# Kernel optimization log

Hardware: AMD Instinct MI355X
Metric: run time of the kernel (lower is better)

## Reference

```python
import jax, jax.numpy as jnp
import numpy as np

B, D, H = 512, 256, 512

def setup_inputs() -> dict:
    key = jax.random.key(0)
    ks = jax.random.split(key, 7)
    s = lambda fan_in: 1.0 / np.sqrt(fan_in)
    return {
        "h": jax.random.normal(ks[0], (B, D), jnp.float32),
        "W1": jax.random.normal(ks[1], (2 * D, H), jnp.float32) * s(2 * D),
        "b1": jax.random.normal(ks[2], (H,), jnp.float32) * s(2 * D),
        "W2": jax.random.normal(ks[3], (H, H), jnp.float32) * s(H),
        "b2": jax.random.normal(ks[4], (H,), jnp.float32) * s(H),
        "W3": jax.random.normal(ks[5], (H, 1), jnp.float32) * s(H),
        "b3": jax.random.normal(ks[6], (1,), jnp.float32) * s(H),
    }

def reference(h, W1, b1, W2, b2, W3, b3):
    n = h.shape[0]
    # Split W1 into halves acting on hi and hj; equivalent to cat([hi,hj]) @ W1
    yi = h @ W1[:D]            # [B, H]
    yj = h @ W1[D:]            # [B, H]
    x = jnp.tanh(yi[:, None, :] + yj[None, :, :] + b1)   # [B, B, H]
    x = jnp.tanh(x @ W2 + b2)                             # [B, B, H]
    logits = (x @ W3 + b3)[..., 0]                        # [B, B]
    eye = jnp.eye(n, dtype=logits.dtype)
    return logits * (1.0 - eye) + (-20.0) * eye
```

## Files before the change

kernel.cpp:

```cpp
#include <hip/hip_runtime.h>
#include <hip/hip_bf16.h>
#include <cstdint>


#define NB 512
#define ND 256
#define NH 512
#define C2 2.885390081777927f

typedef int i32x4 __attribute__((ext_vector_type(4)));
typedef int i32x16 __attribute__((ext_vector_type(16)));
typedef unsigned int u32;
typedef unsigned char u8;

__device__ __forceinline__ float exp2_fast(float x) {
#if __has_builtin(__builtin_amdgcn_exp2f)
  return __builtin_amdgcn_exp2f(x);
#else
  return exp2f(x);
#endif
}
__device__ __forceinline__ float rcp_fast(float x) {
#if __has_builtin(__builtin_amdgcn_rcpf)
  return __builtin_amdgcn_rcpf(x);
#else
  return 1.0f / x;
#endif
}
__device__ __forceinline__ float tanh_pre(float u) {
  return fmaf(-2.0f, rcp_fast(exp2_fast(u) + 1.0f), 1.0f);
}
__device__ __forceinline__ int tanh_q127(float u) {
  return (int)rintf(fmaf(-254.0f, rcp_fast(exp2_fast(u) + 1.0f), 127.0f));
}

__global__ __launch_bounds__(256) void prep_all(const float* __restrict__ h,
                                                const float* __restrict__ W1,
                                                const float* __restrict__ b1,
                                                const float* __restrict__ W2,
                                                float* __restrict__ Ai,
                                                float* __restrict__ Aj,
                                                u8* __restrict__ W2q) {
  const int t = threadIdx.x;
  if (blockIdx.x < 128) {
    __shared__ float hs[4][ND];
    const int i0 = blockIdx.x * 4;
    for (int idx = t; idx < 4 * ND; idx += 256) hs[idx >> 8][idx & 255] = h[i0 * ND + idx];
    __syncthreads();
    float ai0[4] = {0, 0, 0, 0}, ai1[4] = {0, 0, 0, 0};
    float aj0[4] = {0, 0, 0, 0}, aj1[4] = {0, 0, 0, 0};
#pragma unroll 4
    for (int d = 0; d < ND; ++d) {
      const float wA0 = W1[d * NH + t];
      const float wA1 = W1[d * NH + t + 256];
      const float wB0 = W1[(d + ND) * NH + t];
      const float wB1 = W1[(d + ND) * NH + t + 256];
#pragma unroll
      for (int r = 0; r < 4; ++r) {
        const float hd = hs[r][d];
        ai0[r] = fmaf(hd, wA0, ai0[r]);
        ai1[r] = fmaf(hd, wA1, ai1[r]);
        aj0[r] = fmaf(hd, wB0, aj0[r]);
        aj1[r] = fmaf(hd, wB1, aj1[r]);
      }
    }
    const float b1a = b1[t], b1b = b1[t + 256];
#pragma unroll
    for (int r = 0; r < 4; ++r) {
      const int i = i0 + r;
      Ai[i * NH + t] = ai0[r] * C2;
      Ai[i * NH + t + 256] = ai1[r] * C2;
      Aj[i * NH + t] = (aj0[r] + b1a) * C2;
      Aj[i * NH + t + 256] = (aj1[r] + b1b) * C2;
    }
  } else {
    const int g = (blockIdx.x - 128) * 256 + t;
    const int lane = g & 63;
    const int nt = (g >> 6) & 15;
    const int ks = g >> 10;
    const int n = nt * 32 + (lane & 31);
    const int kb = ks * 32 + ((lane >> 5) << 4);
    u32 w[4];
#pragma unroll
    for (int q = 0; q < 4; ++q) {
      u32 acc = 0;
#pragma unroll
      for (int j = 0; j < 4; ++j) {
        const float wv = fminf(fmaxf(W2[(kb + q * 4 + j) * NH + n], -0.25f), 0.25f);
        const int qi = (int)rintf(wv * 508.0f);
        acc |= ((u32)(qi & 255)) << (8 * j);
      }
      w[q] = acc;
    }
    ((uint4*)W2q)[g] = make_uint4(w[0], w[1], w[2], w[3]);
  }
}

__global__ __launch_bounds__(512, 4) void pair_main(const float* __restrict__ Ai,
                                                    const float* __restrict__ Aj,
                                                    const u8* __restrict__ W2q,
                                                    const float* __restrict__ b2,
                                                    const float* __restrict__ W3,
                                                    const float* __restrict__ b3,
                                                    float* __restrict__ out) {
  __shared__ __align__(16) u8 xs[64 * 512];
  __shared__ float red[8][32];

  const int t = threadIdx.x;
  const int w = t >> 6;
  const int lane = t & 63;
  const int lhi = lane >> 5;
  const int llo = lane & 31;
  const int mt = w >> 2;
  const int ng = w & 3;
  const int bx = blockIdx.x;
  const int i = bx >> 3;
  const int j0 = (bx & 7) * 64;

  i32x16 acc[4];
#pragma unroll
  for (int nt = 0; nt < 4; ++nt)
#pragma unroll
    for (int q = 0; q < 16; ++q) acc[nt][q] = 0;

  {
    const float* ajr = Aj + (size_t)(j0 + lane) * NH;
    const float* air = Ai + (size_t)i * NH;
#pragma unroll
    for (int u = 0; u < 4; ++u) {
      const int s = w + u * 8;
      const int k0 = s * 16;
      u32 pk[4];
#pragma unroll
      for (int q = 0; q < 4; ++q) {
        const float4 fa = *(const float4*)(ajr + k0 + q * 4);
        const float4 ga = *(const float4*)(air + k0 + q * 4);
        const int q0 = tanh_q127(fa.x + ga.x);
        const int q1 = tanh_q127(fa.y + ga.y);
        const int q2 = tanh_q127(fa.z + ga.z);
        const int q3 = tanh_q127(fa.w + ga.w);
        pk[q] = ((u32)(q0 & 255)) | ((u32)(q1 & 255) << 8) |
                ((u32)(q2 & 255) << 16) | ((u32)(q3 & 255) << 24);
      }
      ((uint4*)xs)[s * 64 + lane] = make_uint4(pk[0], pk[1], pk[2], pk[3]);
    }
  }
  __syncthreads();

  const i32x4* xsv = (const i32x4*)xs;
  const int aslot = lhi * 64 + mt * 32 + llo;
  const uint4* w2v = (const uint4*)W2q + ng * 256 + lane;

  i32x4 a = xsv[aslot];
  uint4 b0 = w2v[0], b1 = w2v[64], b2r = w2v[128], b3r = w2v[192];

#pragma unroll 2
  for (int ks = 0; ks < 16; ++ks) {
    i32x4 na;
    uint4 nb0, nb1, nb2, nb3;
    if (ks < 15) {
      na = xsv[(ks + 1) * 128 + aslot];
      const uint4* wp = w2v + (ks + 1) * 1024;
      nb0 = wp[0]; nb1 = wp[64]; nb2 = wp[128]; nb3 = wp[192];
    }
    acc[0] = __builtin_amdgcn_mfma_i32_32x32x32_i8(a, __builtin_bit_cast(i32x4, b0), acc[0], 0, 0, 0);
    acc[1] = __builtin_amdgcn_mfma_i32_32x32x32_i8(a, __builtin_bit_cast(i32x4, b1), acc[1], 0, 0, 0);
    acc[2] = __builtin_amdgcn_mfma_i32_32x32x32_i8(a, __builtin_bit_cast(i32x4, b2r), acc[2], 0, 0, 0);
    acc[3] = __builtin_amdgcn_mfma_i32_32x32x32_i8(a, __builtin_bit_cast(i32x4, b3r), acc[3], 0, 0, 0);
    a = na;
    b0 = nb0; b1 = nb1; b2r = nb2; b3r = nb3;
  }

  const float SCALE = (0.25f / (127.0f * 127.0f)) * C2;
  float b2c[4], w3v[4];
#pragma unroll
  for (int ntl = 0; ntl < 4; ++ntl) {
    const int n = ng * 128 + ntl * 32 + llo;
    b2c[ntl] = b2[n] * C2;
    w3v[ntl] = W3[n];
  }
#pragma unroll
  for (int reg = 0; reg < 16; ++reg) {
    float s = 0.0f;
#pragma unroll
    for (int ntl = 0; ntl < 4; ++ntl)
      s += tanh_pre(fmaf((float)acc[ntl][reg], SCALE, b2c[ntl])) * w3v[ntl];
#pragma unroll
    for (int off = 1; off < 32; off <<= 1) s += __shfl_xor(s, off, 64);
    const int row = (reg & 3) + 8 * (reg >> 2) + 4 * lhi;
    if (llo == reg) red[w][row] = s;
  }
  __syncthreads();
  if (t < 64) {
    const int g0 = (t >> 5) * 4;
    const int r = t & 31;
    const float v = red[g0][r] + red[g0 + 1][r] + red[g0 + 2][r] + red[g0 + 3][r] + b3[0];
    const int j = j0 + t;
    out[i * NB + j] = (j == i) ? -20.0f : v;
  }
}

extern "C" void kernel_launch(void* const* d_in, const int* in_sizes, int n_in,
                              void* d_out, int out_size, void* d_ws, size_t ws_size,
                              hipStream_t stream) {
  const float* h = (const float*)d_in[0];
  const float* W1 = (const float*)d_in[1];
  const float* b1 = (const float*)d_in[2];
  const float* W2 = (const float*)d_in[3];
  const float* b2 = (const float*)d_in[4];
  const float* W3 = (const float*)d_in[5];
  const float* b3 = (const float*)d_in[6];
  float* out = (float*)d_out;

  float* Ai = (float*)d_ws;
  float* Aj = Ai + NB * NH;
  u8* W2q = (u8*)(Aj + NB * NH);

  prep_all<<<192, 256, 0, stream>>>(h, W1, b1, W2, Ai, Aj, W2q);
  pair_main<<<4096, 512, 0, stream>>>(Ai, Aj, W2q, b2, W3, b3, out);
}
```

Baseline: 268.8 us.

## Shrink pair tile to 32 rows, magic-number int8 packing, folded tanh epilogue

The main kernel now handles 32 j-rows per block instead of 64, with each of 8 waves owning 64 output columns. That halves LDS use and allows 6 blocks per CU, at the cost of reloading W2q twice as often. The int8 quantization of tanh uses a float magic-constant add plus byte-permute packing instead of rint and shifts. The epilogue folds the constant part of tanh into a precomputed sum of W3, and W2 fragments are double-buffered two steps ahead. The prep kernel also splits its W1 projection across twice as many blocks.

```diff
diff --git a/kernel.cpp b/kernel.cpp
--- a/kernel.cpp
+++ b/kernel.cpp
@@ -27,11 +27,22 @@
   return 1.0f / x;
 #endif
 }
-__device__ __forceinline__ float tanh_pre(float u) {
-  return fmaf(-2.0f, rcp_fast(exp2_fast(u) + 1.0f), 1.0f);
-}
-__device__ __forceinline__ int tanh_q127(float u) {
-  return (int)rintf(fmaf(-254.0f, rcp_fast(exp2_fast(u) + 1.0f), 127.0f));
+__device__ __forceinline__ u32 perm_b32(u32 hi, u32 lo, u32 sel) {
+#if __has_builtin(__builtin_amdgcn_perm)
+  return __builtin_amdgcn_perm(hi, lo, sel);
+#else
+  u32 r = 0;
+  for (int b = 0; b < 4; ++b) {
+    const u32 c = (sel >> (8 * b)) & 255;
+    const u32 byte = (c < 4) ? (lo >> (8 * c)) & 255 : (c < 8) ? (hi >> (8 * (c - 4))) & 255 : 0;
+    r |= byte << (8 * b);
+  }
+  return r;
+#endif
+}
+__device__ __forceinline__ u32 tanh_q127_magic(float u) {
+  const float r = rcp_fast(exp2_fast(u) + 1.0f);
+  return __builtin_bit_cast(u32, fmaf(-254.0f, r, 12583039.0f));
 }
 
 __global__ __launch_bounds__(256) void prep_all(const float* __restrict__ h,
@@ -42,39 +53,33 @@
                                                 float* __restrict__ Aj,
                                                 u8* __restrict__ W2q) {
   const int t = threadIdx.x;
-  if (blockIdx.x < 128) {
+  const int bx = blockIdx.x;
+  if (bx < 256) {
     __shared__ float hs[4][ND];
-    const int i0 = blockIdx.x * 4;
+    const int i0 = (bx >> 1) * 4;
+    const int n = (bx & 1) * 256 + t;
     for (int idx = t; idx < 4 * ND; idx += 256) hs[idx >> 8][idx & 255] = h[i0 * ND + idx];
     __syncthreads();
-    float ai0[4] = {0, 0, 0, 0}, ai1[4] = {0, 0, 0, 0};
-    float aj0[4] = {0, 0, 0, 0}, aj1[4] = {0, 0, 0, 0};
-#pragma unroll 4
+    float ai[4] = {0, 0, 0, 0}, aj[4] = {0, 0, 0, 0};
+#pragma unroll 8
     for (int d = 0; d < ND; ++d) {
-      const float wA0 = W1[d * NH + t];
-      const float wA1 = W1[d * NH + t + 256];
-      const float wB0 = W1[(d + ND) * NH + t];
-      const float wB1 = W1[(d + ND) * NH + t + 256];
+      const float wA = W1[d * NH + n];
+      const float wB = W1[(d + ND) * NH + n];
 #pragma unroll
       for (int r = 0; r < 4; ++r) {
         const float hd = hs[r][d];
-        ai0[r] = fmaf(hd, wA0, ai0[r]);
-        ai1[r] = fmaf(hd, wA1, ai1[r]);
-        aj0[r] = fmaf(hd, wB0, aj0[r]);
-        aj1[r] = fmaf(hd, wB1, aj1[r]);
+        ai[r] = fmaf(hd, wA, ai[r]);
+        aj[r] = fmaf(hd, wB, aj[r]);
       }
     }
-    const float b1a = b1[t], b1b = b1[t + 256];
+    const float b1n = b1[n];
 #pragma unroll
     for (int r = 0; r < 4; ++r) {
-      const int i = i0 + r;
-      Ai[i * NH + t] = ai0[r] * C2;
-      Ai[i * NH + t + 256] = ai1[r] * C2;
-      Aj[i * NH + t] = (aj0[r] + b1a) * C2;
-      Aj[i * NH + t + 256] = (aj1[r] + b1b) * C2;
+      Ai[(i0 + r) * NH + n] = ai[r] * C2;
+      Aj[(i0 + r) * NH + n] = (aj[r] + b1n) * C2;
     }
   } else {
-    const int g = (blockIdx.x - 128) * 256 + t;
+    const int g = (bx - 256) * 256 + t;
     const int lane = g & 63;
     const int nt = (g >> 6) & 15;
     const int ks = g >> 10;
@@ -96,14 +101,14 @@
   }
 }
 
-__global__ __launch_bounds__(512, 4) void pair_main(const float* __restrict__ Ai,
+__global__ __launch_bounds__(512, 6) void pair_main(const float* __restrict__ Ai,
                                                     const float* __restrict__ Aj,
                                                     const u8* __restrict__ W2q,
                                                     const float* __restrict__ b2,
                                                     const float* __restrict__ W3,
                                                     const float* __restrict__ b3,
                                                     float* __restrict__ out) {
-  __shared__ __align__(16) u8 xs[64 * 512];
+  __shared__ __align__(16) u8 xs[32 * 512];
   __shared__ float red[8][32];
 
   const int t = threadIdx.x;
@@ -111,90 +116,99 @@
   const int lane = t & 63;
   const int lhi = lane >> 5;
   const int llo = lane & 31;
-  const int mt = w >> 2;
-  const int ng = w & 3;
   const int bx = blockIdx.x;
-  const int i = bx >> 3;
-  const int j0 = (bx & 7) * 64;
-
-  i32x16 acc[4];
-#pragma unroll
-  for (int nt = 0; nt < 4; ++nt)
+  const int i = bx >> 4;
+  const int j0 = (bx & 15) * 32;
+
+  i32x16 acc[2];
+#pragma unroll
+  for (int nt = 0; nt < 2; ++nt)
 #pragma unroll
     for (int q = 0; q < 16; ++q) acc[nt][q] = 0;
 
   {
-    const float* ajr = Aj + (size_t)(j0 + lane) * NH;
+    const int row = t & 31;
+    const int s0 = t >> 5;
+    const float* ajr = Aj + (size_t)(j0 + row) * NH;
     const float* air = Ai + (size_t)i * NH;
 #pragma unroll
-    for (int u = 0; u < 4; ++u) {
-      const int s = w + u * 8;
+    for (int uu = 0; uu < 2; ++uu) {
+      const int s = s0 + uu * 16;
       const int k0 = s * 16;
-      u32 pk[4];
+      u32 wds[4];
 #pragma unroll
       for (int q = 0; q < 4; ++q) {
         const float4 fa = *(const float4*)(ajr + k0 + q * 4);
         const float4 ga = *(const float4*)(air + k0 + q * 4);
-        const int q0 = tanh_q127(fa.x + ga.x);
-        const int q1 = tanh_q127(fa.y + ga.y);
-        const int q2 = tanh_q127(fa.z + ga.z);
-        const int q3 = tanh_q127(fa.w + ga.w);
-        pk[q] = ((u32)(q0 & 255)) | ((u32)(q1 & 255) << 8) |
-                ((u32)(q2 & 255) << 16) | ((u32)(q3 & 255) << 24);
+        const u32 m0 = tanh_q127_magic(fa.x + ga.x);
+        const u32 m1 = tanh_q127_magic(fa.y + ga.y);
+        const u32 m2 = tanh_q127_magic(fa.z + ga.z);
+        const u32 m3 = tanh_q127_magic(fa.w + ga.w);
+        const u32 p01 = perm_b32(m1, m0, 0x0C0C0400u);
+        const u32 p23 = perm_b32(m3, m2, 0x0C0C0400u);
+        wds[q] = perm_b32(p23, p01, 0x05040100u);
       }
-      ((uint4*)xs)[s * 64 + lane] = make_uint4(pk[0], pk[1], pk[2], pk[3]);
+      ((uint4*)xs)[s * 32 + row] = make_uint4(wds[0], wds[1], wds[2], wds[3]);
     }
   }
   __syncthreads();
 
   const i32x4* xsv = (const i32x4*)xs;
-  const int aslot = lhi * 64 + mt * 32 + llo;
-  const uint4* w2v = (const uint4*)W2q + ng * 256 + lane;
-
-  i32x4 a = xsv[aslot];
-  uint4 b0 = w2v[0], b1 = w2v[64], b2r = w2v[128], b3r = w2v[192];
-
-#pragma unroll 2
+  const int abase = lhi * 32 + llo;
+  const uint4* w2v = (const uint4*)W2q + w * 128 + lane;
+
+  i32x4 a = xsv[abase];
+  uint4 b00 = w2v[0], b01 = w2v[64];
+  uint4 b10 = w2v[1024], b11 = w2v[1024 + 64];
+
+#pragma unroll 4
   for (int ks = 0; ks < 16; ++ks) {
-    i32x4 na;
-    uint4 nb0, nb1, nb2, nb3;
-    if (ks < 15) {
-      na = xsv[(ks + 1) * 128 + aslot];
-      const uint4* wp = w2v + (ks + 1) * 1024;
-      nb0 = wp[0]; nb1 = wp[64]; nb2 = wp[128]; nb3 = wp[192];
-    }
-    acc[0] = __builtin_amdgcn_mfma_i32_32x32x32_i8(a, __builtin_bit_cast(i32x4, b0), acc[0], 0, 0, 0);
-    acc[1] = __builtin_amdgcn_mfma_i32_32x32x32_i8(a, __builtin_bit_cast(i32x4, b1), acc[1], 0, 0, 0);
-    acc[2] = __builtin_amdgcn_mfma_i32_32x32x32_i8(a, __builtin_bit_cast(i32x4, b2r), acc[2], 0, 0, 0);
-    acc[3] = __builtin_amdgcn_mfma_i32_32x32x32_i8(a, __builtin_bit_cast(i32x4, b3r), acc[3], 0, 0, 0);
+    uint4 nb0 = make_uint4(0, 0, 0, 0), nb1 = nb0;
+    i32x4 na = {0, 0, 0, 0};
+    if (ks < 14) {
+      const uint4* wp = w2v + (ks + 2) * 1024;
+      nb0 = wp[0];
+      nb1 = wp[64];
+    }
+    if (ks < 15) na = xsv[(ks + 1) * 64 + abase];
+    acc[0] = __builtin_amdgcn_mfma_i32_32x32x32_i8(a, __builtin_bit_cast(i32x4, b00), acc[0], 0, 0, 0);
+    acc[1] = __builtin_amdgcn_mfma_i32_32x32x32_i8(a, __builtin_bit_cast(i32x4, b01), acc[1], 0, 0, 0);
     a = na;
-    b0 = nb0; b1 = nb1; b2r = nb2; b3r = nb3;
+    b00 = b10; b01 = b11;
+    b10 = nb0; b11 = nb1;
   }
 
   const float SCALE = (0.25f / (127.0f * 127.0f)) * C2;
-  float b2c[4], w3v[4];
-#pragma unroll
-  for (int ntl = 0; ntl < 4; ++ntl) {
-    const int n = ng * 128 + ntl * 32 + llo;
+  float b2c[2], w3v[2];
+#pragma unroll
+  for (int ntl = 0; ntl < 2; ++ntl) {
+    const int n = w * 64 + ntl * 32 + llo;
     b2c[ntl] = b2[n] * C2;
     w3v[ntl] = W3[n];
   }
+  float w3s = w3v[0] + w3v[1];
+#pragma unroll
+  for (int off = 1; off < 32; off <<= 1) w3s += __shfl_xor(w3s, off, 64);
+
 #pragma unroll
   for (int reg = 0; reg < 16; ++reg) {
-    float s = 0.0f;
-#pragma unroll
-    for (int ntl = 0; ntl < 4; ++ntl)
-      s += tanh_pre(fmaf((float)acc[ntl][reg], SCALE, b2c[ntl])) * w3v[ntl];
-#pragma unroll
-    for (int off = 1; off < 32; off <<= 1) s += __shfl_xor(s, off, 64);
+    float sr = 0.0f;
+#pragma unroll
+    for (int ntl = 0; ntl < 2; ++ntl) {
+      const float y = fmaf((float)acc[ntl][reg], SCALE, b2c[ntl]);
+      const float r = rcp_fast(exp2_fast(y) + 1.0f);
+      sr = fmaf(w3v[ntl], r, sr);
+    }
+#pragma unroll
+    for (int off = 1; off < 32; off <<= 1) sr += __shfl_xor(sr, off, 64);
     const int row = (reg & 3) + 8 * (reg >> 2) + 4 * lhi;
-    if (llo == reg) red[w][row] = s;
+    if (llo == reg) red[w][row] = fmaf(-2.0f, sr, w3s);
   }
   __syncthreads();
-  if (t < 64) {
-    const int g0 = (t >> 5) * 4;
-    const int r = t & 31;
-    const float v = red[g0][r] + red[g0 + 1][r] + red[g0 + 2][r] + red[g0 + 3][r] + b3[0];
+  if (t < 32) {
+    float v = b3[0];
+#pragma unroll
+    for (int ww = 0; ww < 8; ++ww) v += red[ww][t];
     const int j = j0 + t;
     out[i * NB + j] = (j == i) ? -20.0f : v;
   }
@@ -216,6 +230,6 @@
   float* Aj = Ai + NB * NH;
   u8* W2q = (u8*)(Aj + NB * NH);
 
-  prep_all<<<192, 256, 0, stream>>>(h, W1, b1, W2, Ai, Aj, W2q);
-  pair_main<<<4096, 512, 0, stream>>>(Ai, Aj, W2q, b2, W3, b3, out);
-}
+  prep_all<<<320, 256, 0, stream>>>(h, W1, b1, W2, Ai, Aj, W2q);
+  pair_main<<<8192, 512, 0, stream>>>(Ai, Aj, W2q, b2, W3, b3, out);
+}
```

Result: faster. 251.9 us (-6.3%).
